# Kernel optimization log

Hardware: AMD Instinct MI355X
Metric: run time of the kernel (lower is better)

The kernel has to match this reference:

```python
import jax, jax.numpy as jnp
import numpy as np

B, L, H, NH = 32, 512, 512, 8
HD = H // NH
SCALE = HD ** -0.5


def _heads(x):
    # (B, L, H) -> (B, NH, L, HD)
    return x.reshape(B, L, NH, HD).transpose(0, 2, 1, 3)


def _score(x, Wq, bq, Wk, bk):
    Q = _heads(x @ Wq.T + bq)
    K = _heads(x @ Wk.T + bk)
    return jnp.einsum('bhqd,bhkd->bhqk', Q, K) * SCALE


def setup_inputs() -> dict:
    key = jax.random.key(0)
    ks = jax.random.split(key, 16)
    d = {
        'seq_id': jax.random.normal(ks[0], (B, L, H), jnp.float32),
        'side_cate': jax.random.normal(ks[1], (B, L, H), jnp.float32),
        'side_brand': jax.random.normal(ks[2], (B, L, H), jnp.float32),
        'V_id_input': jax.random.normal(ks[3], (B, L, H), jnp.float32),
        'relative_time': jax.random.normal(ks[4], (B, NH, L, L), jnp.float32) * 0.02,
        'attn_mask': jnp.broadcast_to(jnp.tril(jnp.ones((L, L), bool)), (B, L, L)),
    }
    s = (2.0 / H) ** 0.5
    names = ['q_id', 'k_id', 'v', 'q_cate', 'k_cate', 'q_brand', 'k_brand', 'o']
    for i, n in enumerate(names):
        d['W' + n] = jax.random.normal(ks[5 + i], (H, H), jnp.float32) * s
        d['b' + n] = jnp.zeros((H,), jnp.float32)
    return d


def reference(seq_id, side_cate, side_brand, V_id_input, relative_time, attn_mask,
              Wq_id, bq_id, Wk_id, bk_id, Wv, bv,
              Wq_cate, bq_cate, Wk_cate, bk_cate,
              Wq_brand, bq_brand, Wk_brand, bk_brand,
              Wo, bo):
    V = _heads(V_id_input @ Wv.T + bv)  # (B, NH, L, HD)
    total = _score(seq_id, Wq_id, bq_id, Wk_id, bk_id)
    total = total + _score(side_cate, Wq_cate, bq_cate, Wk_cate, bk_cate)
    total = total + _score(side_brand, Wq_brand, bq_brand, Wk_brand, bk_brand)
    total = total + relative_time
    total = jnp.where(attn_mask[:, None], total, -jnp.inf)
    w = jax.nn.softmax(total.astype(jnp.float32), axis=-1).astype(total.dtype)
    w = jnp.nan_to_num(w, nan=0.0)
    # eval mode: dropout is identity
    attn_out = jnp.einsum('bhqk,bhkd->bhqd', w, V)
    attn_out = attn_out.transpose(0, 2, 1, 3).reshape(B, L, H)
    return attn_out @ Wo.T + bo
```

## Files before the change

kernel.cpp:

```cpp
#include <hip/hip_runtime.h>
#include <hip/hip_bf16.h>
#include <stdint.h>


typedef __bf16 bf16x8 __attribute__((ext_vector_type(8)));
typedef float f32x4 __attribute__((ext_vector_type(4)));

#define LOG2E 1.4426950408889634f

__device__ int g_isf32;
__device__ __align__(16) unsigned short g_Wbf[8 * 512 * 512];
__device__ __align__(16) unsigned short g_Xbv[32 * 512 * 512];

__device__ __forceinline__ f32x4 mfma16(bf16x8 a, bf16x8 b, f32x4 c) {
    return __builtin_amdgcn_mfma_f32_16x16x32_bf16(a, b, c, 0, 0, 0);
}

__device__ __forceinline__ float qmax16(float x) {
    x = fmaxf(x, __shfl_xor(x, 1));
    x = fmaxf(x, __shfl_xor(x, 2));
    x = fmaxf(x, __shfl_xor(x, 4));
    x = fmaxf(x, __shfl_xor(x, 8));
    return x;
}
__device__ __forceinline__ float qsum16(float x) {
    x += __shfl_xor(x, 1);
    x += __shfl_xor(x, 2);
    x += __shfl_xor(x, 4);
    x += __shfl_xor(x, 8);
    return x;
}

__device__ __forceinline__ float ldf(const void* p, size_t off, int isf) {
    return isf ? ((const float*)p)[off]
               : __bfloat162float(((const __hip_bfloat16*)p)[off]);
}

__device__ __forceinline__ void glds16(const void* g, void* l) {
    __builtin_amdgcn_global_load_lds(
        (const __attribute__((address_space(1))) void*)g,
        (__attribute__((address_space(3))) void*)l, 16, 0, 0);
}

__global__ void sniff_kernel(const unsigned short* __restrict__ p) {
    int t = threadIdx.x;
    int bad = 0, zc = 0;
    #pragma unroll
    for (int i = 0; i < 32; i++) {
        unsigned short u = p[(t * 32 + i) * 2];
        int e = (u >> 7) & 0xFF;
        bad |= (e >= 0xF0);
        zc += (u == 0);
    }
    unsigned long long mb = __ballot(bad != 0);
    #pragma unroll
    for (int s = 1; s < 64; s <<= 1) zc += __shfl_xor(zc, s);
    if (t == 0) g_isf32 = (mb != 0ull || zc > 1024) ? 1 : 0;
}

__global__ __launch_bounds__(256) void conv_all(
    const float* __restrict__ s0, const float* __restrict__ s1,
    const float* __restrict__ s2, const float* __restrict__ s3,
    const float* __restrict__ W0, const float* __restrict__ W1,
    const float* __restrict__ W2, const float* __restrict__ W3,
    const float* __restrict__ W4, const float* __restrict__ W5,
    const float* __restrict__ W6, const float* __restrict__ W7,
    __hip_bfloat16* __restrict__ d0, __hip_bfloat16* __restrict__ d1,
    __hip_bfloat16* __restrict__ d2)
{
    if (!g_isf32) return;
    const int z = blockIdx.z;
    if (z == 4) {
        const int wi = blockIdx.x >> 7;
        const float* src;
        switch (wi) {
            case 0: src = W0; break; case 1: src = W1; break;
            case 2: src = W2; break; case 3: src = W3; break;
            case 4: src = W4; break; case 5: src = W5; break;
            case 6: src = W6; break; default: src = W7; break;
        }
        int i = (blockIdx.x & 127) * 256 + threadIdx.x;
        f32x4 a = ((const f32x4*)src)[2 * i];
        f32x4 b = ((const f32x4*)src)[2 * i + 1];
        bf16x8 o;
        o[0] = (__bf16)a[0]; o[1] = (__bf16)a[1]; o[2] = (__bf16)a[2]; o[3] = (__bf16)a[3];
        o[4] = (__bf16)b[0]; o[5] = (__bf16)b[1]; o[6] = (__bf16)b[2]; o[7] = (__bf16)b[3];
        ((bf16x8*)g_Wbf)[wi * 32768 + i] = o;
        return;
    }
    const float* s = (z == 0) ? s0 : (z == 1) ? s1 : (z == 2) ? s2 : s3;
    __hip_bfloat16* d = (z == 0) ? d0 : (z == 1) ? d1 : (z == 2) ? d2
                                      : (__hip_bfloat16*)g_Xbv;
    const int N8 = 32 * 512 * 512 / 8;
    for (int i = blockIdx.x * 256 + threadIdx.x; i < N8; i += gridDim.x * 256) {
        f32x4 a = ((const f32x4*)s)[2 * i];
        f32x4 b = ((const f32x4*)s)[2 * i + 1];
        bf16x8 o;
        o[0] = (__bf16)a[0]; o[1] = (__bf16)a[1]; o[2] = (__bf16)a[2]; o[3] = (__bf16)a[3];
        o[4] = (__bf16)b[0]; o[5] = (__bf16)b[1]; o[6] = (__bf16)b[2]; o[7] = (__bf16)b[3];
        ((bf16x8*)d)[i] = o;
    }
}

__global__ __launch_bounds__(256, 3) void gemm_all(
    const void* __restrict__ xs, const void* __restrict__ xc,
    const void* __restrict__ xb, const void* __restrict__ xv,
    const __hip_bfloat16* __restrict__ Xbs, const __hip_bfloat16* __restrict__ Xbc,
    const __hip_bfloat16* __restrict__ Xbb,
    const void* __restrict__ W0, const void* __restrict__ B0,
    const void* __restrict__ W1, const void* __restrict__ B1,
    const void* __restrict__ W2, const void* __restrict__ B2,
    const void* __restrict__ W3, const void* __restrict__ B3,
    const void* __restrict__ W4, const void* __restrict__ B4,
    const void* __restrict__ W5, const void* __restrict__ B5,
    const void* __restrict__ W6, const void* __restrict__ B6,
    const void* __restrict__ Wo, const void* __restrict__ Bo,
    const __hip_bfloat16* __restrict__ AO,
    __hip_bfloat16* __restrict__ Qcat, __hip_bfloat16* __restrict__ Kcat,
    __hip_bfloat16* __restrict__ Vt, void* __restrict__ Out,
    int oproj)
{
    __shared__ __align__(16) __hip_bfloat16 As[128 * 64];
    __shared__ __align__(16) __hip_bfloat16 Bs[128 * 64];

    const int isf = g_isf32;
    const int t = threadIdx.x;
    const int lane = t & 63, w = t >> 6;
    const int ln = lane & 15, hi = lane >> 4;
    const int wm = w >> 1, wn = w & 1;
    const int tm = blockIdx.x * 128, tn = blockIdx.y * 128;

    const __hip_bfloat16* Ab;
    const void *W, *bias;
    int kind = 3, comp = 0, wslot = 7;
    if (oproj) {
        Ab = AO; W = Wo; bias = Bo;
    } else {
        switch (blockIdx.z) {
            case 0:  Ab = isf ? Xbs : (const __hip_bfloat16*)xs;
                     W = W0; bias = B0; kind = 0; comp = 0; wslot = 0; break;
            case 1:  Ab = isf ? Xbs : (const __hip_bfloat16*)xs;
                     W = W1; bias = B1; kind = 1; comp = 0; wslot = 1; break;
            case 2:  Ab = isf ? (const __hip_bfloat16*)g_Xbv : (const __hip_bfloat16*)xv;
                     W = W2; bias = B2; kind = 2; comp = 0; wslot = 2; break;
            case 3:  Ab = isf ? Xbc : (const __hip_bfloat16*)xc;
                     W = W3; bias = B3; kind = 0; comp = 1; wslot = 3; break;
            case 4:  Ab = isf ? Xbc : (const __hip_bfloat16*)xc;
                     W = W4; bias = B4; kind = 1; comp = 1; wslot = 4; break;
            case 5:  Ab = isf ? Xbb : (const __hip_bfloat16*)xb;
                     W = W5; bias = B5; kind = 0; comp = 2; wslot = 5; break;
            default: Ab = isf ? Xbb : (const __hip_bfloat16*)xb;
                     W = W6; bias = B6; kind = 1; comp = 2; wslot = 6; break;
        }
    }
    const __hip_bfloat16* Wb = isf ? (const __hip_bfloat16*)g_Wbf + (size_t)wslot * 262144
                                   : (const __hip_bfloat16*)W;

    const int csw = (((lane & 7) ^ ((lane >> 3) & 7)) * 8);
    const int rsub = (w * 8) + (lane >> 3);

    f32x4 acc[4][4] = {};

    for (int k0 = 0; k0 < 512; k0 += 64) {
        #pragma unroll
        for (int r = 0; r < 4; r++)
            glds16(Ab + (size_t)(tm + r * 32 + rsub) * 512 + k0 + csw,
                   (char*)As + r * 4096 + w * 1024);
        #pragma unroll
        for (int r = 0; r < 4; r++)
            glds16(Wb + (size_t)(tn + r * 32 + rsub) * 512 + k0 + csw,
                   (char*)Bs + r * 4096 + w * 1024);
        __syncthreads();

        #pragma unroll
        for (int kk = 0; kk < 64; kk += 32) {
            bf16x8 af[4], bfr[4];
            #pragma unroll
            for (int i = 0; i < 4; i++)
                af[i] = *(const bf16x8*)&As[(wm * 64 + i * 16 + ln) * 64 +
                                            ((kk + hi * 8) ^ ((ln & 7) * 8))];
            #pragma unroll
            for (int j = 0; j < 4; j++)
                bfr[j] = *(const bf16x8*)&Bs[(wn * 64 + j * 16 + ln) * 64 +
                                             ((kk + hi * 8) ^ ((ln & 7) * 8))];
            #pragma unroll
            for (int i = 0; i < 4; i++)
                #pragma unroll
                for (int j = 0; j < 4; j++)
                    acc[i][j] = mfma16(af[i], bfr[j], acc[i][j]);
        }
        __syncthreads();
    }

    #pragma unroll
    for (int j = 0; j < 4; j++) {
        int col = tn + wn * 64 + j * 16 + ln;
        float bv = ldf(bias, col, isf);
        int h = col >> 6, d = col & 63;
        #pragma unroll
        for (int i = 0; i < 4; i++) {
            #pragma unroll
            for (int r = 0; r < 4; r++) {
                int row = tm + wm * 64 + i * 16 + hi * 4 + r;
                float val = acc[i][j][r] + bv;
                int b = row >> 9, l = row & 511;
                if (kind == 0)
                    Qcat[((size_t)(b * 8 + h) * 512 + l) * 192 + comp * 64 + d] =
                        __float2bfloat16(val);
                else if (kind == 1)
                    Kcat[((size_t)(b * 8 + h) * 512 + l) * 192 + comp * 64 + d] =
                        __float2bfloat16(val);
                else if (kind == 2)
                    Vt[((size_t)(b * 8 + h) * 64 + d) * 512 + l] =
                        __float2bfloat16(val);
                else if (isf)
                    ((float*)Out)[(size_t)row * 512 + col] = val;
                else
                    ((__hip_bfloat16*)Out)[(size_t)row * 512 + col] =
                        __float2bfloat16(val);
            }
        }
    }
}

__global__ __launch_bounds__(256, 2) void attn_kernel(
    const __hip_bfloat16* __restrict__ Qcat,
    const __hip_bfloat16* __restrict__ Kcat,
    const __hip_bfloat16* __restrict__ Vt,
    const void* __restrict__ rel,
    __hip_bfloat16* __restrict__ AO)
{
    __shared__ __align__(16) __hip_bfloat16 Ks[64 * 200];
    __shared__ __align__(16) __hip_bfloat16 Vs[64 * 72];
    __shared__ __align__(16) __hip_bfloat16 Ps[4 * 32 * 72];

    const int isf = g_isf32;
    const int t = threadIdx.x;
    const int lane = t & 63, w = t >> 6;
    const int ln = lane & 15, hi = lane >> 4;
    const int qt = blockIdx.x, h = blockIdx.y, b = blockIdx.z;
    const int qb = qt * 128;
    const size_t bh = (size_t)(b * 8 + h);

    const __hip_bfloat16* qc = Qcat + bh * 512 * 192;
    const __hip_bfloat16* kc = Kcat + bh * 512 * 192;
    const __hip_bfloat16* vp = Vt + bh * 64 * 512;
    const size_t rbase = bh * 512 * 512;

    bf16x8 qf[2][6];
    #pragma unroll
    for (int i = 0; i < 2; i++)
        #pragma unroll
        for (int kf = 0; kf < 6; kf++)
            qf[i][kf] = *(const bf16x8*)(qc + (size_t)(qb + w * 32 + i * 16 + ln) * 192
                                            + kf * 32 + hi * 8);

    float mst[2][4], lst[2][4];
    f32x4 oacc[2][4] = {};
    #pragma unroll
    for (int i = 0; i < 2; i++)
        #pragma unroll
        for (int r = 0; r < 4; r++) { mst[i][r] = -1e30f; lst[i][r] = 0.f; }

    const int nkt = 2 * qt + 2;
    for (int kt = 0; kt < nkt; kt++) {
        const int kb = kt * 64;
        __syncthreads();

        #pragma unroll
        for (int r = 0; r < 6; r++) {
            int e = r * 2048 + t * 8;
            int row = e / 192, col = e - row * 192;
            bf16x8 v = *(const bf16x8*)(kc + (size_t)(kb + row) * 192 + col);
            *(bf16x8*)&Ks[row * 200 + col] = v;
        }
        #pragma unroll
        for (int r = 0; r < 2; r++) {
            int e = r * 2048 + t * 8;
            int row = e >> 6, col = e & 63;
            bf16x8 v = *(const bf16x8*)(vp + (size_t)row * 512 + kb + col);
            *(bf16x8*)&Vs[row * 72 + col] = v;
        }
        __syncthreads();

        f32x4 s[2][4] = {};
        __builtin_amdgcn_s_setprio(1);
        #pragma unroll
        for (int kf = 0; kf < 6; kf++) {
            bf16x8 bfr[4];
            #pragma unroll
            for (int j = 0; j < 4; j++)
                bfr[j] = *(const bf16x8*)&Ks[(j * 16 + ln) * 200 + kf * 32 + hi * 8];
            #pragma unroll
            for (int i = 0; i < 2; i++)
                #pragma unroll
                for (int j = 0; j < 4; j++)
                    s[i][j] = mfma16(qf[i][kf], bfr[j], s[i][j]);
        }
        __builtin_amdgcn_s_setprio(0);

        #pragma unroll
        for (int i = 0; i < 2; i++) {
            #pragma unroll
            for (int r = 0; r < 4; r++) {
                int qrow = qb + w * 32 + i * 16 + hi * 4 + r;
                size_t roff = rbase + (size_t)qrow * 512 + kb;
                #pragma unroll
                for (int j = 0; j < 4; j++) {
                    int col = kb + j * 16 + ln;
                    float rv = ldf(rel, roff + j * 16 + ln, isf);
                    float v = fmaf(s[i][j][r], 0.125f * LOG2E, rv * LOG2E);
                    s[i][j][r] = (col > qrow) ? -1e30f : v;
                }
            }
        }

        #pragma unroll
        for (int i = 0; i < 2; i++) {
            #pragma unroll
            for (int r = 0; r < 4; r++) {
                float mx = fmaxf(fmaxf(s[i][0][r], s[i][1][r]),
                                 fmaxf(s[i][2][r], s[i][3][r]));
                mx = qmax16(mx);
                float mnew = fmaxf(mst[i][r], mx);
                float al = exp2f(mst[i][r] - mnew);
                float sum = 0.f;
                #pragma unroll
                for (int j = 0; j < 4; j++) {
                    float p = exp2f(s[i][j][r] - mnew);
                    s[i][j][r] = p;
                    sum += p;
                }
                sum = qsum16(sum);
                lst[i][r] = lst[i][r] * al + sum;
                mst[i][r] = mnew;
                #pragma unroll
                for (int jn = 0; jn < 4; jn++)
                    oacc[i][jn][r] *= al;
            }
        }

        __hip_bfloat16* pw = &Ps[w * 32 * 72];
        #pragma unroll
        for (int i = 0; i < 2; i++) {
            #pragma unroll
            for (int r = 0; r < 4; r++) {
                int prow = i * 16 + hi * 4 + r;
                #pragma unroll
                for (int j = 0; j < 4; j++)
                    pw[prow * 72 + j * 16 + ln] = __float2bfloat16(s[i][j][r]);
            }
        }
        __syncthreads();

        __builtin_amdgcn_s_setprio(1);
        #pragma unroll
        for (int kk = 0; kk < 64; kk += 32) {
            bf16x8 ap[2], bv[4];
            #pragma unroll
            for (int i = 0; i < 2; i++)
                ap[i] = *(const bf16x8*)&Ps[w * 2304 + (i * 16 + ln) * 72 + kk + hi * 8];
            #pragma unroll
            for (int jn = 0; jn < 4; jn++)
                bv[jn] = *(const bf16x8*)&Vs[(jn * 16 + ln) * 72 + kk + hi * 8];
            #pragma unroll
            for (int i = 0; i < 2; i++)
                #pragma unroll
                for (int jn = 0; jn < 4; jn++)
                    oacc[i][jn] = mfma16(ap[i], bv[jn], oacc[i][jn]);
        }
        __builtin_amdgcn_s_setprio(0);
    }

    #pragma unroll
    for (int i = 0; i < 2; i++) {
        #pragma unroll
        for (int r = 0; r < 4; r++) {
            int qrow = qb + w * 32 + i * 16 + hi * 4 + r;
            float inv = 1.0f / lst[i][r];
            __hip_bfloat16* orow = AO + ((size_t)(b * 512 + qrow)) * 512 + h * 64;
            #pragma unroll
            for (int jn = 0; jn < 4; jn++)
                orow[jn * 16 + ln] = __float2bfloat16(oacc[i][jn][r] * inv);
        }
    }
}

extern "C" void kernel_launch(void* const* d_in, const int* in_sizes, int n_in,
                              void* d_out, int out_size, void* d_ws, size_t ws_size,
                              hipStream_t stream) {
    (void)in_sizes; (void)n_in; (void)out_size; (void)ws_size;
    const void* xs  = d_in[0];
    const void* xc  = d_in[1];
    const void* xb  = d_in[2];
    const void* xv  = d_in[3];
    const void* rel = d_in[4];
    const void* W0 = d_in[6];    const void* B0 = d_in[7];
    const void* W1 = d_in[8];    const void* B1 = d_in[9];
    const void* W2 = d_in[10];   const void* B2 = d_in[11];
    const void* W3 = d_in[12];   const void* B3 = d_in[13];
    const void* W4 = d_in[14];   const void* B4 = d_in[15];
    const void* W5 = d_in[16];   const void* B5 = d_in[17];
    const void* W6 = d_in[18];   const void* B6 = d_in[19];
    const void* Wo = d_in[20];   const void* Bo = d_in[21];

    char* ws = (char*)d_ws;
    __hip_bfloat16* Qcat = (__hip_bfloat16*)(ws);
    __hip_bfloat16* Kcat = (__hip_bfloat16*)(ws + 50331648);
    __hip_bfloat16* Vt   = (__hip_bfloat16*)(ws + 100663296);
    __hip_bfloat16* AO   = (__hip_bfloat16*)(ws + 117440512);

    __hip_bfloat16* Xbs = AO;
    __hip_bfloat16* Xbc = (__hip_bfloat16*)d_out;
    __hip_bfloat16* Xbb = (__hip_bfloat16*)((char*)d_out + 16777216);

    dim3 blk(256, 1, 1);
    sniff_kernel<<<1, 64, 0, stream>>>((const unsigned short*)xs);
    conv_all<<<dim3(1024, 1, 5), blk, 0, stream>>>(
        (const float*)xs, (const float*)xc, (const float*)xb, (const float*)xv,
        (const float*)W0, (const float*)W1, (const float*)W2, (const float*)W3,
        (const float*)W4, (const float*)W5, (const float*)W6, (const float*)Wo,
        Xbs, Xbc, Xbb);
    gemm_all<<<dim3(128, 4, 7), blk, 0, stream>>>(
        xs, xc, xb, xv, Xbs, Xbc, Xbb,
        W0, B0, W1, B1, W2, B2, W3, B3, W4, B4, W5, B5, W6, B6,
        Wo, Bo, AO, Qcat, Kcat, Vt, d_out, 0);
    attn_kernel<<<dim3(4, 8, 32), blk, 0, stream>>>(Qcat, Kcat, Vt, rel, AO);
    gemm_all<<<dim3(128, 4, 1), blk, 0, stream>>>(
        xs, xc, xb, xv, Xbs, Xbc, Xbb,
        W0, B0, W1, B1, W2, B2, W3, B3, W4, B4, W5, B5, W6, B6,
        Wo, Bo, AO, Qcat, Kcat, Vt, d_out, 1);
}
```

Baseline: 682.8 us.

## Load K/V fragments directly from global, drop block syncs, per-wave causal bounds

The attention kernel no longer stages K and V tiles in shared memory. Each wave reads its MFMA B-operand fragments straight from global memory, which removes all block-wide barriers from the key loop. Because waves no longer share tiles, each wave can stop at its own causal bound (2*qt + w/2 + 1 tiles), skipping fully masked key tiles. Query tiles are also scheduled in reverse so the heaviest blocks launch first. The cost is that the four waves re-read K/V redundantly through the cache, and the per-wave P writes to Ps now rely on wave-local ordering without a barrier.

New measurement: 725.1 us. 1.06x slower.

```diff
diff --git a/kernel.cpp b/kernel.cpp
--- a/kernel.cpp
+++ b/kernel.cpp
@@ -230,15 +230,14 @@
     const void* __restrict__ rel,
     __hip_bfloat16* __restrict__ AO)
 {
-    __shared__ __align__(16) __hip_bfloat16 Ks[64 * 200];
-    __shared__ __align__(16) __hip_bfloat16 Vs[64 * 72];
     __shared__ __align__(16) __hip_bfloat16 Ps[4 * 32 * 72];
 
     const int isf = g_isf32;
     const int t = threadIdx.x;
     const int lane = t & 63, w = t >> 6;
     const int ln = lane & 15, hi = lane >> 4;
-    const int qt = blockIdx.x, h = blockIdx.y, b = blockIdx.z;
+    const int qt = 3 - blockIdx.x;
+    const int h = blockIdx.y, b = blockIdx.z;
     const int qb = qt * 128;
     const size_t bh = (size_t)(b * 8 + h);
 
@@ -262,26 +261,9 @@
         #pragma unroll
         for (int r = 0; r < 4; r++) { mst[i][r] = -1e30f; lst[i][r] = 0.f; }
 
-    const int nkt = 2 * qt + 2;
+    const int nkt = 2 * qt + (w >> 1) + 1;
     for (int kt = 0; kt < nkt; kt++) {
         const int kb = kt * 64;
-        __syncthreads();
-
-        #pragma unroll
-        for (int r = 0; r < 6; r++) {
-            int e = r * 2048 + t * 8;
-            int row = e / 192, col = e - row * 192;
-            bf16x8 v = *(const bf16x8*)(kc + (size_t)(kb + row) * 192 + col);
-            *(bf16x8*)&Ks[row * 200 + col] = v;
-        }
-        #pragma unroll
-        for (int r = 0; r < 2; r++) {
-            int e = r * 2048 + t * 8;
-            int row = e >> 6, col = e & 63;
-            bf16x8 v = *(const bf16x8*)(vp + (size_t)row * 512 + kb + col);
-            *(bf16x8*)&Vs[row * 72 + col] = v;
-        }
-        __syncthreads();
 
         f32x4 s[2][4] = {};
         __builtin_amdgcn_s_setprio(1);
@@ -290,7 +272,8 @@
             bf16x8 bfr[4];
             #pragma unroll
             for (int j = 0; j < 4; j++)
-                bfr[j] = *(const bf16x8*)&Ks[(j * 16 + ln) * 200 + kf * 32 + hi * 8];
+                bfr[j] = *(const bf16x8*)(kc + (size_t)(kb + j * 16 + ln) * 192
+                                             + kf * 32 + hi * 8);
             #pragma unroll
             for (int i = 0; i < 2; i++)
                 #pragma unroll
@@ -351,7 +334,6 @@
                     pw[prow * 72 + j * 16 + ln] = __float2bfloat16(s[i][j][r]);
             }
         }
-        __syncthreads();
 
         __builtin_amdgcn_s_setprio(1);
         #pragma unroll
@@ -362,7 +344,8 @@
                 ap[i] = *(const bf16x8*)&Ps[w * 2304 + (i * 16 + ln) * 72 + kk + hi * 8];
             #pragma unroll
             for (int jn = 0; jn < 4; jn++)
-                bv[jn] = *(const bf16x8*)&Vs[(jn * 16 + ln) * 72 + kk + hi * 8];
+                bv[jn] = *(const bf16x8*)(vp + (size_t)(jn * 16 + ln) * 512
+                                             + kb + kk + hi * 8);
             #pragma unroll
             for (int i = 0; i < 2; i++)
                 #pragma unroll
```
